# Kernel tuning notes

Hardware: AMD Instinct MI355X
Metric: run time of the kernel (lower is better)

## Reference

```python
import jax, jax.numpy as jnp
import numpy as np

N, E, L, HID, HEADS, G = 50000, 800000, 2, 128, 8, 256
DK = HID // HEADS

def _ln(x, g, b, eps=1e-5):
    m = jnp.mean(x, axis=-1, keepdims=True)
    v = jnp.mean((x - m) ** 2, axis=-1, keepdims=True)
    return (x - m) * jax.lax.rsqrt(v + eps) * g + b

def setup_inputs() -> dict:
    key = jax.random.key(0)
    ks = jax.random.split(key, 24)
    rn = lambda i, s: (0.05 * jax.random.normal(ks[i], s)).astype(jnp.float32)
    return {
        'node_attr': jax.random.randint(ks[0], (N, 4), 0, 64, dtype=jnp.int32),
        'batch_idx': jnp.sort(jax.random.randint(ks[1], (N,), 0, G, dtype=jnp.int32)),
        'edge_index': jax.random.randint(ks[2], (2, E), 0, N, dtype=jnp.int32),
        'strat_dist': jax.random.randint(ks[3], (E,), 0, 32, dtype=jnp.int32),
        'strat_path': jax.random.randint(ks[4], (E,), 0, 16, dtype=jnp.int32),
        'atom_emb': rn(5, (4, 64, HID)),
        'dist_emb': rn(6, (L, 32, HID)),
        'path_emb': rn(7, (L, 16, HID)),
        'Wq': rn(8, (L, HID, HID)), 'bq': rn(9, (L, HID)),
        'Wk': rn(10, (L, HID, HID)), 'bk': rn(11, (L, HID)),
        'Wv': rn(12, (L, HID, HID)), 'bv': rn(13, (L, HID)),
        'Wa': rn(14, (L, HID, HID)), 'ba': rn(15, (L, HID)),
        'ln1_g': jnp.ones((L, HID), jnp.float32), 'ln1_b': jnp.zeros((L, HID), jnp.float32),
        'Wmid': rn(16, (L, HID, 2 * HID)), 'bmid': rn(17, (L, 2 * HID)),
        'Wo': rn(18, (L, 2 * HID, HID)), 'bo': rn(19, (L, HID)),
        'ln2_g': jnp.ones((L, HID), jnp.float32), 'ln2_b': jnp.zeros((L, HID), jnp.float32),
        'W_out': rn(20, (HID, 1)), 'b_out': jnp.zeros((1,), jnp.float32),
    }

def reference(node_attr, batch_idx, edge_index, strat_dist, strat_path,
              atom_emb, dist_emb, path_emb, Wq, bq, Wk, bk, Wv, bv, Wa, ba,
              ln1_g, ln1_b, Wmid, bmid, Wo, bo, ln2_g, ln2_b, W_out, b_out):
    # node encoder: sum of per-feature embeddings (AtomEncoder style)
    x = sum(atom_emb[f][node_attr[:, f]] for f in range(node_attr.shape[1]))  # [N, HID]
    src, tgt = edge_index[0], edge_index[1]  # j (source), i (target)
    inv_sqrt_dk = np.float32(1.0 / np.sqrt(DK))
    for l in range(L):
        # per-edge gather + relational encodings added to the source vector
        s = x[src] + dist_emb[l][strat_dist] + path_emb[l][strat_path]  # [E, HID]
        t = x[tgt]                                                      # [E, HID]
        q = (t @ Wq[l] + bq[l]).reshape(E, HEADS, DK)
        k = (s @ Wk[l] + bk[l]).reshape(E, HEADS, DK)
        v = (s @ Wv[l] + bv[l]).reshape(E, HEADS, DK)
        scores = jnp.sum(q * k, axis=-1) * inv_sqrt_dk  # [E, HEADS]
        # segment softmax keyed on target node id
        smax = jax.ops.segment_max(scores, tgt, num_segments=N)
        ex = jnp.exp(scores - smax[tgt])
        den = jax.ops.segment_sum(ex, tgt, num_segments=N)
        att = ex / (den[tgt] + 1e-16)                   # [E, HEADS]
        msg = (v * att[:, :, None]).reshape(E, HID)
        aggr = jax.ops.segment_sum(msg, tgt, num_segments=N)  # scatter-add
        # update: attn FFN + residual + LayerNorms (dropout is identity in eval)
        h = _ln(jax.nn.gelu(aggr, approximate=False) @ Wa[l] + ba[l] + x, ln1_g[l], ln1_b[l])
        h2 = jax.nn.gelu(h @ Wmid[l] + bmid[l], approximate=False) @ Wo[l] + bo[l]
        x = _ln(h2 + h, ln2_g[l], ln2_b[l])
    # global mean pool per graph, then readout
    cnt = jax.ops.segment_sum(jnp.ones((N,), x.dtype), batch_idx, num_segments=G)
    pooled = jax.ops.segment_sum(x, batch_idx, num_segments=G) / jnp.maximum(cnt, 1.0)[:, None]
    return pooled @ W_out + b_out
```

## Files before the change

kernel.cpp:

```cpp
#include <hip/hip_runtime.h>
#include <hip/hip_bf16.h>
#include <math.h>
#include <stdint.h>

#define N_NODES 50000
#define N_EDGES 800000
#define HID 128
#define NGRAPH 256
#define NLAYER 2
#define CAP 64

#define SC_GRP 196
#define SC_B (SC_GRP * 8)
#define NPART 6250

#define ENC_B 3125
#define TKV_B (ENC_B + 1024)
#define RPK_B (TKV_B + 128)
#define PREP_B (RPK_B + 4)

#define PKE_B 782
#define PKZ_B 196
#define PACK_B (PKE_B + PKZ_B)

typedef __bf16 bf16x8 __attribute__((ext_vector_type(8)));
typedef __bf16 bf16x4 __attribute__((ext_vector_type(4)));
typedef __bf16 bf16x2 __attribute__((ext_vector_type(2)));
typedef float f32x4 __attribute__((ext_vector_type(4)));
typedef float f32x2 __attribute__((ext_vector_type(2)));

__device__ __forceinline__ float gelu_f(float v) {
    return 0.5f * v * (1.0f + erff(v * 0.70710678118654752f));
}

__device__ __forceinline__ f32x2 f8lo(uint32_t d) {
    return __builtin_amdgcn_cvt_pk_f32_fp8((int)d, false);
}
__device__ __forceinline__ f32x2 f8hi(uint32_t d) {
    return __builtin_amdgcn_cvt_pk_f32_fp8((int)d, true);
}
__device__ __forceinline__ uint32_t pk4_fp8(float a, float b, float c, float d) {
    int w = __builtin_amdgcn_cvt_pk_fp8_f32(a, b, 0, false);
    w = __builtin_amdgcn_cvt_pk_fp8_f32(c, d, w, true);
    return (uint32_t)w;
}
__device__ __forceinline__ f32x2 bfpair(uint32_t d) {
    f32x2 r;
    r[0] = __uint_as_float(d << 16);
    r[1] = __uint_as_float(d);
    return r;
}

__global__ __launch_bounds__(256) void pack_kernel(
    const int* __restrict__ tgt, const int* __restrict__ src,
    const int* __restrict__ sd, const int* __restrict__ sp,
    uint32_t* __restrict__ pack, uint16_t* __restrict__ t16,
    int* __restrict__ cnt) {
    int b = blockIdx.x;
    int tid = threadIdx.x;
    if (b < PKE_B) {
        int e0 = b * 1024 + tid * 4;
        if (e0 + 3 < N_EDGES) {
            int4 s4 = *(const int4*)(src + e0);
            int4 d4 = *(const int4*)(sd + e0);
            int4 p4 = *(const int4*)(sp + e0);
            int4 t4 = *(const int4*)(tgt + e0);
            uint4 o;
            o.x = (uint32_t)s4.x | ((uint32_t)((d4.x << 4) | p4.x) << 16);
            o.y = (uint32_t)s4.y | ((uint32_t)((d4.y << 4) | p4.y) << 16);
            o.z = (uint32_t)s4.z | ((uint32_t)((d4.z << 4) | p4.z) << 16);
            o.w = (uint32_t)s4.w | ((uint32_t)((d4.w << 4) | p4.w) << 16);
            *(uint4*)(pack + e0) = o;
            uint2 tt;
            tt.x = (uint32_t)t4.x | ((uint32_t)t4.y << 16);
            tt.y = (uint32_t)t4.z | ((uint32_t)t4.w << 16);
            *(uint2*)(t16 + e0) = tt;
        }
    } else {
        int idx = (b - PKE_B) * 256 + tid;
        if (idx < N_NODES) cnt[idx] = 0;
    }
}

__global__ __launch_bounds__(256) void prep_kernel(
    const int* __restrict__ attr, const float* __restrict__ aemb,
    __bf16* __restrict__ xb,
    const float* __restrict__ de, const float* __restrict__ pe,
    const float* __restrict__ Wk, const float* __restrict__ Wv,
    __bf16* __restrict__ tkv,
    const float* __restrict__ Wq, const float* __restrict__ Wa,
    const float* __restrict__ Wmid, const float* __restrict__ Wo,
    __bf16* __restrict__ wqkvf, __bf16* __restrict__ waf,
    __bf16* __restrict__ wmidf, __bf16* __restrict__ wof,
    const int* __restrict__ batch, const float* __restrict__ bout,
    const float* __restrict__ bq, const float* __restrict__ bk,
    const float* __restrict__ bv,
    float* __restrict__ invc, float* __restrict__ outp, float* __restrict__ bqkv,
    const uint16_t* __restrict__ t16, const uint32_t* __restrict__ pack,
    int* __restrict__ cnt, uint32_t* __restrict__ ei) {
    __shared__ float sde[128];
    int b = blockIdx.x;
    int tid = threadIdx.x;
    if (b < SC_B) {
        int grp = b >> 3;
        int part = b & 7;
        unsigned plo = (unsigned)(part * NPART);
        int base = grp * 4096 + tid;
#pragma unroll
        for (int k = 0; k < 16; k++) {
            int e = base + k * 256;
            if (e < N_EDGES) {
                unsigned tl = (unsigned)t16[e] - plo;
                if (tl < (unsigned)NPART) {
                    int t = (int)(tl + plo);
                    uint32_t pk = pack[e];
                    int r = atomicAdd(&cnt[t], 1);
                    if (r < CAP) ei[(t << 6) + r] = pk;
                }
            }
        }
        return;
    }
    b -= SC_B;
    if (b < ENC_B) {
        int gid = b * 256 + tid;
        int n = gid >> 4;
        int c8 = (gid & 15) << 3;
        const int4 a = *(const int4*)(attr + n * 4);
        const float* r0 = aemb + (size_t)(0 * 64 + a.x) * 128 + c8;
        const float* r1 = aemb + (size_t)(1 * 64 + a.y) * 128 + c8;
        const float* r2 = aemb + (size_t)(2 * 64 + a.z) * 128 + c8;
        const float* r3 = aemb + (size_t)(3 * 64 + a.w) * 128 + c8;
        f32x4 v0a = *(const f32x4*)r0, v0b = *(const f32x4*)(r0 + 4);
        f32x4 v1a = *(const f32x4*)r1, v1b = *(const f32x4*)(r1 + 4);
        f32x4 v2a = *(const f32x4*)r2, v2b = *(const f32x4*)(r2 + 4);
        f32x4 v3a = *(const f32x4*)r3, v3b = *(const f32x4*)(r3 + 4);
        bf16x8 o;
#pragma unroll
        for (int j = 0; j < 4; j++) {
            o[j] = (__bf16)(v0a[j] + v1a[j] + v2a[j] + v3a[j]);
            o[4 + j] = (__bf16)(v0b[j] + v1b[j] + v2b[j] + v3b[j]);
        }
        *(bf16x8*)(xb + (size_t)n * 128 + c8) = o;
    } else if (b < TKV_B) {
        int bb = b - ENC_B;
        int l = bb >> 9;
        int md = bb & 511;
        int dd = md >> 4, pp = md & 15;
        int c = tid;
        if (c < 128) sde[c] = de[l * 4096 + dd * 128 + c] + pe[l * 2048 + pp * 128 + c];
        __syncthreads();
        const float* W = (c < 128) ? (Wk + l * 16384) : (Wv + l * 16384);
        int cc = c & 127;
        float acc = 0.f;
#pragma unroll 4
        for (int k = 0; k < 128; k++) acc = fmaf(sde[k], W[k * 128 + cc], acc);
        tkv[(size_t)bb * 256 + c] = (__bf16)acc;
    } else if (b < RPK_B) {
        int u = (b - TKV_B) * 256 + tid;
        int l = u >> 14, r = u & 16383;
        const float* srcp;
        __bf16* dstp;
        int kg, scol, srcCO;
        if (r < 6144) {
            kg = r / 384;
            int uu = r % 384;
            int sec = uu >> 7, cc = uu & 127;
            scol = ((cc & 15) << 3) | (cc >> 4);
            const float* Ws = (sec == 0) ? Wq : (sec == 1) ? Wk : Wv;
            srcp = Ws + l * 16384;
            srcCO = 128;
            dstp = wqkvf + (size_t)l * 49152 + (size_t)r * 8;
        } else if (r < 8192) {
            int rr = r - 6144;
            kg = rr >> 7;
            int cc = rr & 127;
            scol = ((cc & 15) << 3) | (cc >> 4);
            srcp = Wa + l * 16384;
            srcCO = 128;
            dstp = waf + (size_t)l * 16384 + (size_t)rr * 8;
        } else if (r < 12288) {
            int rr = r - 8192;
            kg = rr >> 8;
            int uu = rr & 255;
            int blk = uu >> 7, cc = uu & 127;
            scol = blk * 128 + (((cc & 15) << 3) | (cc >> 4));
            srcp = Wmid + l * 32768;
            srcCO = 256;
            dstp = wmidf + (size_t)l * 32768 + (size_t)rr * 8;
        } else {
            int rr = r - 12288;
            kg = rr >> 7;
            int cc = rr & 127;
            scol = ((cc & 15) << 3) | (cc >> 4);
            srcp = Wo + l * 32768;
            srcCO = 128;
            dstp = wof + (size_t)l * 32768 + (size_t)rr * 8;
        }
        bf16x8 o;
#pragma unroll
        for (int j = 0; j < 8; j++) o[j] = (__bf16)srcp[(kg * 8 + j) * srcCO + scol];
        *(bf16x8*)dstp = o;
    } else {
        int sb = b - RPK_B;
        if (sb == 0) {
            int g = tid;
            int lo = 0, hi = N_NODES;
            while (lo < hi) { int mid = (lo + hi) >> 1; if (batch[mid] < g) lo = mid + 1; else hi = mid; }
            int start = lo;
            lo = start; hi = N_NODES;
            while (lo < hi) { int mid = (lo + hi) >> 1; if (batch[mid] < g + 1) lo = mid + 1; else hi = mid; }
            int c2 = lo - start;
            invc[g] = 1.0f / fmaxf((float)c2, 1.0f);
            outp[g] = bout[0];
        } else {
            int r = (sb - 1) * 256 + tid;
            int l = r / 384, c = r % 384;
            float v = (c < 128) ? bq[l * 128 + c]
                    : (c < 256) ? bk[l * 128 + c - 128]
                                : bv[l * 128 + c - 256];
            bqkv[r] = v;
        }
    }
}

__global__ __launch_bounds__(256) void qkv_gemm(
    const __bf16* __restrict__ A, const __bf16* __restrict__ Wf,
    const float* __restrict__ bias, __bf16* __restrict__ Qb,
    uint8_t* __restrict__ kv8, int M) {
    int tid = threadIdx.x;
    int bq = blockIdx.x;
    int sec = bq % 3;
    int rowblk = bq / 3;
    int lane = tid & 63;
    int wv = tid >> 6;
    int row0 = rowblk * 64 + wv * 16;
    int col0 = sec * 128;
    if (row0 >= M) return;
    int quad = lane >> 4, tq = lane & 15;
    f32x4 acc[8] = {};
#pragma unroll
    for (int k0 = 0; k0 < 128; k0 += 32) {
        int rr = row0 + tq;
        if (rr >= M) rr = M - 1;
        bf16x8 af = *(const bf16x8*)(A + (size_t)rr * 128 + k0 + quad * 8);
#pragma unroll
        for (int nt = 0; nt < 8; nt++) {
            bf16x8 bfr = *(const bf16x8*)(Wf + ((size_t)((k0 >> 3) + quad) * 384 + col0 + nt * 16 + tq) * 8);
            acc[nt] = __builtin_amdgcn_mfma_f32_16x16x32_bf16(af, bfr, acc[nt], 0, 0, 0);
        }
    }
    int cb = tq * 8;
    float bia[8];
#pragma unroll
    for (int t = 0; t < 8; t++) bia[t] = bias[col0 + cb + t];
#pragma unroll
    for (int v = 0; v < 4; v++) {
        int rr = row0 + quad * 4 + v;
        if (rr >= M) continue;
        float val[8];
#pragma unroll
        for (int t = 0; t < 8; t++) val[t] = acc[t][v] + bia[t];
        if (sec == 0) {
            bf16x8 ov;
#pragma unroll
            for (int t = 0; t < 8; t++) ov[t] = (__bf16)val[t];
            *(bf16x8*)(Qb + (size_t)rr * 128 + cb) = ov;
        } else {
            uint2 st;
            st.x = pk4_fp8(val[0], val[1], val[2], val[3]);
            st.y = pk4_fp8(val[4], val[5], val[6], val[7]);
            *(uint2*)(kv8 + (size_t)rr * 256 + (sec - 1) * 128 + cb) = st;
        }
    }
}

template <bool POOL>
__global__ __launch_bounds__(256) void ffn_uber(
    const __bf16* __restrict__ A,
    const __bf16* __restrict__ xres,
    const __bf16* __restrict__ Waf, const float* __restrict__ ba,
    const float* __restrict__ l1g, const float* __restrict__ l1b,
    const __bf16* __restrict__ Wmf, const float* __restrict__ bmid,
    const __bf16* __restrict__ Wof, const float* __restrict__ bo,
    const float* __restrict__ l2g, const float* __restrict__ l2b,
    __bf16* __restrict__ outx,
    const int* __restrict__ batch, const float* __restrict__ invc,
    const float* __restrict__ WoutV, float* __restrict__ outp,
    int M) {
    __shared__ __bf16 hld[4][16][136];
    __shared__ __bf16 smid[4][16][264];
    __shared__ float ps[POOL ? NGRAPH : 1];
    int lane = threadIdx.x & 63;
    int wv = threadIdx.x >> 6;
    int row0 = blockIdx.x * 64 + wv * 16;
    bool active = row0 < M;
    if (POOL) {
        ps[threadIdx.x] = 0.f;
        __syncthreads();
    } else if (!active) {
        return;
    }
    int quad = lane >> 4, tq = lane & 15;
    if (active) {
        int cb = tq * 8;
        {
            f32x4 acc[8] = {};
#pragma unroll
            for (int k0 = 0; k0 < 128; k0 += 32) {
                int rr = row0 + tq;
                if (rr >= M) rr = M - 1;
                bf16x8 af = *(const bf16x8*)(A + (size_t)rr * 128 + k0 + quad * 8);
#pragma unroll
                for (int nt = 0; nt < 8; nt++) {
                    bf16x8 bfr = *(const bf16x8*)(Waf + ((size_t)((k0 >> 3) + quad) * 128 + nt * 16 + tq) * 8);
                    acc[nt] = __builtin_amdgcn_mfma_f32_16x16x32_bf16(af, bfr, acc[nt], 0, 0, 0);
                }
            }
            float bia[8], gv[8], bv2[8];
#pragma unroll
            for (int t = 0; t < 8; t++) {
                bia[t] = ba[cb + t];
                gv[t] = l1g[cb + t];
                bv2[t] = l1b[cb + t];
            }
#pragma unroll
            for (int v = 0; v < 4; v++) {
                int rr = row0 + quad * 4 + v;
                int rc = (rr < M) ? rr : M - 1;
                bf16x8 rv = *(const bf16x8*)(xres + (size_t)rc * 128 + cb);
                float val[8];
#pragma unroll
                for (int t = 0; t < 8; t++) val[t] = acc[t][v] + bia[t] + (float)rv[t];
                float s = 0.f, s2 = 0.f;
#pragma unroll
                for (int t = 0; t < 8; t++) { s += val[t]; s2 = fmaf(val[t], val[t], s2); }
#pragma unroll
                for (int o = 1; o < 16; o <<= 1) {
                    s += __shfl_xor(s, o);
                    s2 += __shfl_xor(s2, o);
                }
                float m = s * (1.0f / 128.0f);
                float var = s2 * (1.0f / 128.0f) - m * m;
                float rs = rsqrtf(var + 1e-5f);
                bf16x8 ov;
#pragma unroll
                for (int t = 0; t < 8; t++) ov[t] = (__bf16)((val[t] - m) * rs * gv[t] + bv2[t]);
                *(bf16x8*)(&hld[wv][quad * 4 + v][cb]) = ov;
            }
        }
        asm volatile("" ::: "memory");
#pragma unroll
        for (int cH = 0; cH < 2; ++cH) {
            f32x4 acc[8] = {};
#pragma unroll
            for (int k0 = 0; k0 < 128; k0 += 32) {
                bf16x8 af = *(const bf16x8*)(&hld[wv][tq][k0 + quad * 8]);
#pragma unroll
                for (int nt = 0; nt < 8; nt++) {
                    bf16x8 bfr = *(const bf16x8*)(Wmf + ((size_t)((k0 >> 3) + quad) * 256 + cH * 128 + nt * 16 + tq) * 8);
                    acc[nt] = __builtin_amdgcn_mfma_f32_16x16x32_bf16(af, bfr, acc[nt], 0, 0, 0);
                }
            }
            int cb2 = cH * 128 + cb;
            float bia[8];
#pragma unroll
            for (int t = 0; t < 8; t++) bia[t] = bmid[cb2 + t];
#pragma unroll
            for (int v = 0; v < 4; v++) {
                bf16x8 ov;
#pragma unroll
                for (int t = 0; t < 8; t++) ov[t] = (__bf16)gelu_f(acc[t][v] + bia[t]);
                *(bf16x8*)(&smid[wv][quad * 4 + v][cb2]) = ov;
            }
        }
        asm volatile("" ::: "memory");
        f32x4 acc[8] = {};
#pragma unroll
        for (int k0 = 0; k0 < 256; k0 += 32) {
            bf16x8 af = *(const bf16x8*)(&smid[wv][tq][k0 + quad * 8]);
#pragma unroll
            for (int nt = 0; nt < 8; nt++) {
                bf16x8 bfr = *(const bf16x8*)(Wof + ((size_t)((k0 >> 3) + quad) * 128 + nt * 16 + tq) * 8);
                acc[nt] = __builtin_amdgcn_mfma_f32_16x16x32_bf16(af, bfr, acc[nt], 0, 0, 0);
            }
        }
        float bia[8], gv[8], bv2[8], wo8[8];
#pragma unroll
        for (int t = 0; t < 8; t++) {
            bia[t] = bo[cb + t];
            gv[t] = l2g[cb + t];
            bv2[t] = l2b[cb + t];
        }
        if (POOL) {
#pragma unroll
            for (int t = 0; t < 8; t++) wo8[t] = WoutV[cb + t];
        }
#pragma unroll
        for (int v = 0; v < 4; v++) {
            int rr = row0 + quad * 4 + v;
            bf16x8 rv = *(const bf16x8*)(&hld[wv][quad * 4 + v][cb]);
            float val[8];
#pragma unroll
            for (int t = 0; t < 8; t++) val[t] = acc[t][v] + bia[t] + (float)rv[t];
            float s = 0.f, s2 = 0.f;
#pragma unroll
            for (int t = 0; t < 8; t++) { s += val[t]; s2 = fmaf(val[t], val[t], s2); }
#pragma unroll
            for (int o = 1; o < 16; o <<= 1) {
                s += __shfl_xor(s, o);
                s2 += __shfl_xor(s2, o);
            }
            float m = s * (1.0f / 128.0f);
            float var = s2 * (1.0f / 128.0f) - m * m;
            float rs = rsqrtf(var + 1e-5f);
#pragma unroll
            for (int t = 0; t < 8; t++) val[t] = (val[t] - m) * rs * gv[t] + bv2[t];
            if (rr >= M) continue;
            if (!POOL) {
                bf16x8 ov;
#pragma unroll
                for (int t = 0; t < 8; t++) ov[t] = (__bf16)val[t];
                *(bf16x8*)(outx + (size_t)rr * 128 + cb) = ov;
            } else {
                float dot = 0.f;
#pragma unroll
                for (int t = 0; t < 8; t++) dot = fmaf(val[t], wo8[t], dot);
#pragma unroll
                for (int o = 1; o < 16; o <<= 1) dot += __shfl_xor(dot, o);
                if (tq == 0) {
                    int g = batch[rr];
                    atomicAdd(&ps[g], dot * invc[g]);
                }
            }
        }
    }
    if (POOL) {
        __syncthreads();
        float pv = ps[threadIdx.x];
        if (pv != 0.f) atomicAdd(&outp[threadIdx.x], pv);
    }
}

__global__ __launch_bounds__(256) void attn_kernel(
    const __bf16* __restrict__ Qb, const uint8_t* __restrict__ kv8,
    const __bf16* __restrict__ tkv,
    const int* __restrict__ cnt, const uint32_t* __restrict__ ei,
    __bf16* __restrict__ outb) {
    int wv = threadIdx.x >> 6;
    int lane = threadIdx.x & 63;
    int nd = lane >> 5;
    int slot = (lane >> 3) & 3;
    int h = lane & 7;
    int i = blockIdx.x * 8 + wv * 2 + nd;
    int ch0 = h * 16;
    const uint4* qv = (const uint4*)(Qb + (size_t)i * 128 + ch0);
    uint4 qa = qv[0], qb = qv[1];
    uint32_t qd[8] = {qa.x, qa.y, qa.z, qa.w, qb.x, qb.y, qb.z, qb.w};
    f32x2 qp[8];
#pragma unroll
    for (int j = 0; j < 8; j++) qp[j] = bfpair(qd[j]);
    int deg = cnt[i];
    if (deg > CAP) deg = CAP;
    int p0 = i << 6;
    int p1 = p0 + deg;
    float l = 0.f;
    f32x2 ap[8] = {};
    int p = p0 + slot;
    uint32_t w1 = 0, w2 = 0;
    if (p < p1) w1 = ei[p];
    if (p + 4 < p1) w2 = ei[p + 4];
    uint4 kw, vw, t0, t1, u0, u1;
    {
        int j = w1 & 0xffff, md = w1 >> 16;
        const uint8_t* kr = kv8 + (size_t)j * 256 + ch0;
        kw = *(const uint4*)kr;
        vw = *(const uint4*)(kr + 128);
        const __bf16* tr = tkv + md * 256 + ch0;
        t0 = *(const uint4*)tr;
        t1 = *(const uint4*)(tr + 8);
        u0 = *(const uint4*)(tr + 128);
        u1 = *(const uint4*)(tr + 136);
    }
    while (p < p1) {
        uint4 kwn, vwn, t0n, t1n, u0n, u1n;
        {
            int j = w2 & 0xffff, md = w2 >> 16;
            const uint8_t* kr = kv8 + (size_t)j * 256 + ch0;
            kwn = *(const uint4*)kr;
            vwn = *(const uint4*)(kr + 128);
            const __bf16* tr = tkv + md * 256 + ch0;
            t0n = *(const uint4*)tr;
            t1n = *(const uint4*)(tr + 8);
            u0n = *(const uint4*)(tr + 128);
            u1n = *(const uint4*)(tr + 136);
        }
        int pn = p + 8;
        uint32_t w3 = ei[(pn < p1) ? pn : p0];
        uint32_t kd[4] = {kw.x, kw.y, kw.z, kw.w};
        uint32_t vd[4] = {vw.x, vw.y, vw.z, vw.w};
        uint32_t td[8] = {t0.x, t0.y, t0.z, t0.w, t1.x, t1.y, t1.z, t1.w};
        uint32_t ud[8] = {u0.x, u0.y, u0.z, u0.w, u1.x, u1.y, u1.z, u1.w};
        f32x2 sa = {0.f, 0.f};
#pragma unroll
        for (int j = 0; j < 4; j++) {
            f32x2 klo = f8lo(kd[j]) + bfpair(td[2 * j]);
            f32x2 khi = f8hi(kd[j]) + bfpair(td[2 * j + 1]);
            sa = qp[2 * j] * klo + sa;
            sa = qp[2 * j + 1] * khi + sa;
        }
        float s = sa[0] + sa[1];
        float pe = __expf(s * 0.25f);
        l += pe;
        f32x2 pp = {pe, pe};
#pragma unroll
        for (int j = 0; j < 4; j++) {
            f32x2 vlo = f8lo(vd[j]) + bfpair(ud[2 * j]);
            f32x2 vhi = f8hi(vd[j]) + bfpair(ud[2 * j + 1]);
            ap[2 * j] = pp * vlo + ap[2 * j];
            ap[2 * j + 1] = pp * vhi + ap[2 * j + 1];
        }
        kw = kwn; vw = vwn; t0 = t0n; t1 = t1n; u0 = u0n; u1 = u1n;
        w2 = w3;
        p += 4;
    }
#pragma unroll
    for (int m = 8; m <= 16; m <<= 1) {
        l += __shfl_xor(l, m);
#pragma unroll
        for (int j = 0; j < 8; j++) {
            f32x2 o;
            o[0] = __shfl_xor(ap[j][0], m);
            o[1] = __shfl_xor(ap[j][1], m);
            ap[j] = ap[j] + o;
        }
    }
    float inv = 1.0f / (l + 1e-16f);
    f32x2 va = ap[0], vb = ap[1];
    if (slot == 1) { va = ap[2]; vb = ap[3]; }
    if (slot == 2) { va = ap[4]; vb = ap[5]; }
    if (slot == 3) { va = ap[6]; vb = ap[7]; }
    bf16x4 o4;
    o4[0] = (__bf16)gelu_f(va[0] * inv);
    o4[1] = (__bf16)gelu_f(va[1] * inv);
    o4[2] = (__bf16)gelu_f(vb[0] * inv);
    o4[3] = (__bf16)gelu_f(vb[1] * inv);
    *(bf16x4*)(outb + (size_t)i * 128 + ch0 + slot * 4) = o4;
}

extern "C" void kernel_launch(void* const* d_in, const int* in_sizes, int n_in,
                              void* d_out, int out_size, void* d_ws, size_t ws_size,
                              hipStream_t stream) {
    const int N = N_NODES, E = N_EDGES;
    const int* node_attr = (const int*)d_in[0];
    const int* batch_idx = (const int*)d_in[1];
    const int* edge_index = (const int*)d_in[2];
    const int* strat_dist = (const int*)d_in[3];
    const int* strat_path = (const int*)d_in[4];
    const float* atom_emb = (const float*)d_in[5];
    const float* dist_emb = (const float*)d_in[6];
    const float* path_emb = (const float*)d_in[7];
    const float* Wq = (const float*)d_in[8];
    const float* bq = (const float*)d_in[9];
    const float* Wk = (const float*)d_in[10];
    const float* bk = (const float*)d_in[11];
    const float* Wv = (const float*)d_in[12];
    const float* bv = (const float*)d_in[13];
    const float* Wa = (const float*)d_in[14];
    const float* ba = (const float*)d_in[15];
    const float* ln1g = (const float*)d_in[16];
    const float* ln1b = (const float*)d_in[17];
    const float* Wmid = (const float*)d_in[18];
    const float* bmid = (const float*)d_in[19];
    const float* Wo = (const float*)d_in[20];
    const float* bo = (const float*)d_in[21];
    const float* ln2g = (const float*)d_in[22];
    const float* ln2b = (const float*)d_in[23];
    const float* Wout = (const float*)d_in[24];
    const float* bout = (const float*)d_in[25];
    float* out = (float*)d_out;

    const int* src = edge_index;
    const int* tgt = edge_index + E;

    size_t NF = (size_t)N * HID;
    float* invc = (float*)d_ws;
    float* bqkv = invc + 256;
    __bf16* xb = (__bf16*)(bqkv + 768);
    __bf16* Qb = xb + NF;
    __bf16* ab = Qb + NF;
    __bf16* tkv = ab + NF;
    __bf16* wqkvf = tkv + 262144;
    __bf16* waf = wqkvf + 98304;
    __bf16* wmidf = waf + 32768;
    __bf16* wof = wmidf + 65536;
    uint8_t* kv8 = (uint8_t*)(wof + 65536);
    uint32_t* ei = (uint32_t*)(kv8 + (size_t)N * 256);
    int* cnt = (int*)(ei + (size_t)N * CAP);
    uint32_t* pack = (uint32_t*)(cnt + N_NODES);
    uint16_t* t16 = (uint16_t*)(pack + N_EDGES);

    pack_kernel<<<PACK_B, 256, 0, stream>>>(
        tgt, src, strat_dist, strat_path, pack, t16, cnt);
    prep_kernel<<<SC_B + PREP_B, 256, 0, stream>>>(
        node_attr, atom_emb, xb,
        dist_emb, path_emb, Wk, Wv, tkv,
        Wq, Wa, Wmid, Wo, wqkvf, waf, wmidf, wof,
        batch_idx, bout, bq, bk, bv, invc, out, bqkv,
        t16, pack, cnt, ei);

    const int GB = (N + 63) / 64;
    const int AB = (N + 7) / 8;

    for (int l = 0; l < NLAYER; ++l) {
        qkv_gemm<<<3 * GB, 256, 0, stream>>>(
            xb, wqkvf + l * 49152, bqkv + l * 384, Qb, kv8, N);

        attn_kernel<<<AB, 256, 0, stream>>>(Qb, kv8, tkv + l * 131072, cnt, ei, ab);

        if (l < NLAYER - 1) {
            ffn_uber<false><<<GB, 256, 0, stream>>>(
                ab, xb, waf + l * 16384, ba + l * 128, ln1g + l * 128, ln1b + l * 128,
                wmidf + l * 32768, bmid + l * 256, wof + l * 32768, bo + l * 128,
                ln2g + l * 128, ln2b + l * 128, xb,
                nullptr, nullptr, nullptr, nullptr, N);
        } else {
            ffn_uber<true><<<GB, 256, 0, stream>>>(
                ab, xb, waf + l * 16384, ba + l * 128, ln1g + l * 128, ln1b + l * 128,
                wmidf + l * 32768, bmid + l * 256, wof + l * 32768, bo + l * 128,
                ln2g + l * 128, ln2b + l * 128, nullptr,
                batch_idx, invc, Wout, out, N);
        }
    }
}
```

Measured before the change: 412.8 us.

## Assign one wavefront per node in attention with 8 edge slots and butterfly reduce

The attention kernel now maps one 64-lane wavefront to each target node instead of two nodes per wavefront, so 8 edge slots per node are processed in parallel instead of 4. The cross-slot reduction becomes a recursive-halving butterfly that exchanges half the accumulators per step, ending with each lane owning two output channels, which cuts shuffle count. This doubles the grid size and halves the per-lane loop trip count for high-degree nodes, at the cost of more idle lanes on low-degree nodes (average degree is around 16).

```diff
diff --git a/kernel.cpp b/kernel.cpp
--- a/kernel.cpp
+++ b/kernel.cpp
@@ -24,7 +24,6 @@
 #define PACK_B (PKE_B + PKZ_B)
 
 typedef __bf16 bf16x8 __attribute__((ext_vector_type(8)));
-typedef __bf16 bf16x4 __attribute__((ext_vector_type(4)));
 typedef __bf16 bf16x2 __attribute__((ext_vector_type(2)));
 typedef float f32x4 __attribute__((ext_vector_type(4)));
 typedef float f32x2 __attribute__((ext_vector_type(2)));
@@ -48,6 +47,12 @@
     f32x2 r;
     r[0] = __uint_as_float(d << 16);
     r[1] = __uint_as_float(d);
+    return r;
+}
+__device__ __forceinline__ f32x2 shfl2(f32x2 v, int m) {
+    f32x2 r;
+    r[0] = __shfl_xor(v[0], m);
+    r[1] = __shfl_xor(v[1], m);
     return r;
 }
 
@@ -448,11 +453,9 @@
     const int* __restrict__ cnt, const uint32_t* __restrict__ ei,
     __bf16* __restrict__ outb) {
     int wv = threadIdx.x >> 6;
+    int i = blockIdx.x * 4 + wv;
     int lane = threadIdx.x & 63;
-    int nd = lane >> 5;
-    int slot = (lane >> 3) & 3;
-    int h = lane & 7;
-    int i = blockIdx.x * 8 + wv * 2 + nd;
+    int slot = lane >> 3, h = lane & 7;
     int ch0 = h * 16;
     const uint4* qv = (const uint4*)(Qb + (size_t)i * 128 + ch0);
     uint4 qa = qv[0], qb = qv[1];
@@ -469,7 +472,7 @@
     int p = p0 + slot;
     uint32_t w1 = 0, w2 = 0;
     if (p < p1) w1 = ei[p];
-    if (p + 4 < p1) w2 = ei[p + 4];
+    if (p + 8 < p1) w2 = ei[p + 8];
     uint4 kw, vw, t0, t1, u0, u1;
     {
         int j = w1 & 0xffff, md = w1 >> 16;
@@ -495,8 +498,8 @@
             u0n = *(const uint4*)(tr + 128);
             u1n = *(const uint4*)(tr + 136);
         }
-        int pn = p + 8;
-        uint32_t w3 = ei[(pn < p1) ? pn : p0];
+        int pn = p + 16;
+        uint32_t w3 = ei[(pn < p1) ? pn : p];
         uint32_t kd[4] = {kw.x, kw.y, kw.z, kw.w};
         uint32_t vd[4] = {vw.x, vw.y, vw.z, vw.w};
         uint32_t td[8] = {t0.x, t0.y, t0.z, t0.w, t1.x, t1.y, t1.z, t1.w};
@@ -522,30 +525,40 @@
         }
         kw = kwn; vw = vwn; t0 = t0n; t1 = t1n; u0 = u0n; u1 = u1n;
         w2 = w3;
-        p += 4;
-    }
-#pragma unroll
-    for (int m = 8; m <= 16; m <<= 1) {
-        l += __shfl_xor(l, m);
-#pragma unroll
-        for (int j = 0; j < 8; j++) {
-            f32x2 o;
-            o[0] = __shfl_xor(ap[j][0], m);
-            o[1] = __shfl_xor(ap[j][1], m);
-            ap[j] = ap[j] + o;
-        }
+        p += 8;
+    }
+    int b3 = (lane >> 3) & 1, b4 = (lane >> 4) & 1, b5 = lane >> 5;
+    f32x2 k0, k1, k2, k3;
+    {
+        f32x2 s0 = b3 ? ap[0] : ap[1];
+        f32x2 s1 = b3 ? ap[2] : ap[3];
+        f32x2 s2 = b3 ? ap[4] : ap[5];
+        f32x2 s3 = b3 ? ap[6] : ap[7];
+        k0 = (b3 ? ap[1] : ap[0]) + shfl2(s0, 8);
+        k1 = (b3 ? ap[3] : ap[2]) + shfl2(s1, 8);
+        k2 = (b3 ? ap[5] : ap[4]) + shfl2(s2, 8);
+        k3 = (b3 ? ap[7] : ap[6]) + shfl2(s3, 8);
+        l += __shfl_xor(l, 8);
+    }
+    f32x2 m0, m1;
+    {
+        f32x2 s0 = b4 ? k0 : k1;
+        f32x2 s1 = b4 ? k2 : k3;
+        m0 = (b4 ? k1 : k0) + shfl2(s0, 16);
+        m1 = (b4 ? k3 : k2) + shfl2(s1, 16);
+        l += __shfl_xor(l, 16);
+    }
+    f32x2 fin;
+    {
+        f32x2 s0 = b5 ? m0 : m1;
+        fin = (b5 ? m1 : m0) + shfl2(s0, 32);
+        l += __shfl_xor(l, 32);
     }
     float inv = 1.0f / (l + 1e-16f);
-    f32x2 va = ap[0], vb = ap[1];
-    if (slot == 1) { va = ap[2]; vb = ap[3]; }
-    if (slot == 2) { va = ap[4]; vb = ap[5]; }
-    if (slot == 3) { va = ap[6]; vb = ap[7]; }
-    bf16x4 o4;
-    o4[0] = (__bf16)gelu_f(va[0] * inv);
-    o4[1] = (__bf16)gelu_f(va[1] * inv);
-    o4[2] = (__bf16)gelu_f(vb[0] * inv);
-    o4[3] = (__bf16)gelu_f(vb[1] * inv);
-    *(bf16x4*)(outb + (size_t)i * 128 + ch0 + slot * 4) = o4;
+    bf16x2 o2;
+    o2[0] = (__bf16)gelu_f(fin[0] * inv);
+    o2[1] = (__bf16)gelu_f(fin[1] * inv);
+    *(bf16x2*)(outb + (size_t)i * 128 + ch0 + slot * 2) = o2;
 }
 
 extern "C" void kernel_launch(void* const* d_in, const int* in_sizes, int n_in,
@@ -610,7 +623,7 @@
         t16, pack, cnt, ei);
 
     const int GB = (N + 63) / 64;
-    const int AB = (N + 7) / 8;
+    const int AB = (N + 3) / 4;
 
     for (int l = 0; l < NLAYER; ++l) {
         qkv_gemm<<<3 * GB, 256, 0, stream>>>(
```

After: 372.6 us. 1.11x faster.

## Fuse node encoding with layer-0 QKV GEMM and widen attention per-node wave

Applied to the files above, without the earlier changes.

Weight repacking and setup move into the pack kernel. The node encoder now stages each 64-node tile in shared memory and computes the layer-0 Q/K/V projection with MFMA inside the same prep kernel, which removes the first qkv_gemm launch and the re-read of x. The attention kernel now assigns one full wave per target node instead of half a wave, and processes 8 edges per step with an extra shuffle-reduction stage. The ENCQ blocks depend on repacked weights, so the prep kernel must run after the pack kernel. Some encoder blocks now carry heavy GEMM work while the scatter blocks are light, which risks load imbalance.

```diff
diff --git a/kernel.cpp b/kernel.cpp
--- a/kernel.cpp
+++ b/kernel.cpp
@@ -14,17 +14,17 @@
 #define SC_B (SC_GRP * 8)
 #define NPART 6250
 
-#define ENC_B 3125
-#define TKV_B (ENC_B + 1024)
-#define RPK_B (TKV_B + 128)
-#define PREP_B (RPK_B + 4)
+#define ENCQ_B 782
+#define TKV_B 1024
+#define PREPM_B (SC_B + ENCQ_B + TKV_B)
 
 #define PKE_B 782
 #define PKZ_B 196
-#define PACK_B (PKE_B + PKZ_B)
+#define RPK0 (PKE_B + PKZ_B)
+#define SET0 (RPK0 + 128)
+#define PACK_B (SET0 + 4)
 
 typedef __bf16 bf16x8 __attribute__((ext_vector_type(8)));
-typedef __bf16 bf16x4 __attribute__((ext_vector_type(4)));
 typedef __bf16 bf16x2 __attribute__((ext_vector_type(2)));
 typedef float f32x4 __attribute__((ext_vector_type(4)));
 typedef float f32x2 __attribute__((ext_vector_type(2)));
@@ -55,7 +55,16 @@
     const int* __restrict__ tgt, const int* __restrict__ src,
     const int* __restrict__ sd, const int* __restrict__ sp,
     uint32_t* __restrict__ pack, uint16_t* __restrict__ t16,
-    int* __restrict__ cnt) {
+    int* __restrict__ cnt,
+    const float* __restrict__ Wq, const float* __restrict__ Wa,
+    const float* __restrict__ Wmid, const float* __restrict__ Wo,
+    const float* __restrict__ Wk, const float* __restrict__ Wv,
+    __bf16* __restrict__ wqkvf, __bf16* __restrict__ waf,
+    __bf16* __restrict__ wmidf, __bf16* __restrict__ wof,
+    const int* __restrict__ batch, const float* __restrict__ bout,
+    const float* __restrict__ bq, const float* __restrict__ bk,
+    const float* __restrict__ bv,
+    float* __restrict__ invc, float* __restrict__ outp, float* __restrict__ bqkv) {
     int b = blockIdx.x;
     int tid = threadIdx.x;
     if (b < PKE_B) {
@@ -76,88 +85,11 @@
             tt.y = (uint32_t)t4.z | ((uint32_t)t4.w << 16);
             *(uint2*)(t16 + e0) = tt;
         }
-    } else {
+    } else if (b < RPK0) {
         int idx = (b - PKE_B) * 256 + tid;
         if (idx < N_NODES) cnt[idx] = 0;
-    }
-}
-
-__global__ __launch_bounds__(256) void prep_kernel(
-    const int* __restrict__ attr, const float* __restrict__ aemb,
-    __bf16* __restrict__ xb,
-    const float* __restrict__ de, const float* __restrict__ pe,
-    const float* __restrict__ Wk, const float* __restrict__ Wv,
-    __bf16* __restrict__ tkv,
-    const float* __restrict__ Wq, const float* __restrict__ Wa,
-    const float* __restrict__ Wmid, const float* __restrict__ Wo,
-    __bf16* __restrict__ wqkvf, __bf16* __restrict__ waf,
-    __bf16* __restrict__ wmidf, __bf16* __restrict__ wof,
-    const int* __restrict__ batch, const float* __restrict__ bout,
-    const float* __restrict__ bq, const float* __restrict__ bk,
-    const float* __restrict__ bv,
-    float* __restrict__ invc, float* __restrict__ outp, float* __restrict__ bqkv,
-    const uint16_t* __restrict__ t16, const uint32_t* __restrict__ pack,
-    int* __restrict__ cnt, uint32_t* __restrict__ ei) {
-    __shared__ float sde[128];
-    int b = blockIdx.x;
-    int tid = threadIdx.x;
-    if (b < SC_B) {
-        int grp = b >> 3;
-        int part = b & 7;
-        unsigned plo = (unsigned)(part * NPART);
-        int base = grp * 4096 + tid;
-#pragma unroll
-        for (int k = 0; k < 16; k++) {
-            int e = base + k * 256;
-            if (e < N_EDGES) {
-                unsigned tl = (unsigned)t16[e] - plo;
-                if (tl < (unsigned)NPART) {
-                    int t = (int)(tl + plo);
-                    uint32_t pk = pack[e];
-                    int r = atomicAdd(&cnt[t], 1);
-                    if (r < CAP) ei[(t << 6) + r] = pk;
-                }
-            }
-        }
-        return;
-    }
-    b -= SC_B;
-    if (b < ENC_B) {
-        int gid = b * 256 + tid;
-        int n = gid >> 4;
-        int c8 = (gid & 15) << 3;
-        const int4 a = *(const int4*)(attr + n * 4);
-        const float* r0 = aemb + (size_t)(0 * 64 + a.x) * 128 + c8;
-        const float* r1 = aemb + (size_t)(1 * 64 + a.y) * 128 + c8;
-        const float* r2 = aemb + (size_t)(2 * 64 + a.z) * 128 + c8;
-        const float* r3 = aemb + (size_t)(3 * 64 + a.w) * 128 + c8;
-        f32x4 v0a = *(const f32x4*)r0, v0b = *(const f32x4*)(r0 + 4);
-        f32x4 v1a = *(const f32x4*)r1, v1b = *(const f32x4*)(r1 + 4);
-        f32x4 v2a = *(const f32x4*)r2, v2b = *(const f32x4*)(r2 + 4);
-        f32x4 v3a = *(const f32x4*)r3, v3b = *(const f32x4*)(r3 + 4);
-        bf16x8 o;
-#pragma unroll
-        for (int j = 0; j < 4; j++) {
-            o[j] = (__bf16)(v0a[j] + v1a[j] + v2a[j] + v3a[j]);
-            o[4 + j] = (__bf16)(v0b[j] + v1b[j] + v2b[j] + v3b[j]);
-        }
-        *(bf16x8*)(xb + (size_t)n * 128 + c8) = o;
-    } else if (b < TKV_B) {
-        int bb = b - ENC_B;
-        int l = bb >> 9;
-        int md = bb & 511;
-        int dd = md >> 4, pp = md & 15;
-        int c = tid;
-        if (c < 128) sde[c] = de[l * 4096 + dd * 128 + c] + pe[l * 2048 + pp * 128 + c];
-        __syncthreads();
-        const float* W = (c < 128) ? (Wk + l * 16384) : (Wv + l * 16384);
-        int cc = c & 127;
-        float acc = 0.f;
-#pragma unroll 4
-        for (int k = 0; k < 128; k++) acc = fmaf(sde[k], W[k * 128 + cc], acc);
-        tkv[(size_t)bb * 256 + c] = (__bf16)acc;
-    } else if (b < RPK_B) {
-        int u = (b - TKV_B) * 256 + tid;
+    } else if (b < SET0) {
+        int u = (b - RPK0) * 256 + tid;
         int l = u >> 14, r = u & 16383;
         const float* srcp;
         __bf16* dstp;
@@ -202,7 +134,7 @@
         for (int j = 0; j < 8; j++) o[j] = (__bf16)srcp[(kg * 8 + j) * srcCO + scol];
         *(bf16x8*)dstp = o;
     } else {
-        int sb = b - RPK_B;
+        int sb = b - SET0;
         if (sb == 0) {
             int g = tid;
             int lo = 0, hi = N_NODES;
@@ -221,6 +153,127 @@
                                 : bv[l * 128 + c - 256];
             bqkv[r] = v;
         }
+    }
+}
+
+__global__ __launch_bounds__(256) void prep_mega(
+    const int* __restrict__ attr, const float* __restrict__ aemb,
+    __bf16* __restrict__ xb,
+    const float* __restrict__ de, const float* __restrict__ pe,
+    const float* __restrict__ Wk, const float* __restrict__ Wv,
+    __bf16* __restrict__ tkv,
+    const __bf16* __restrict__ wqkvf, const float* __restrict__ bqkv,
+    __bf16* __restrict__ Qb, uint8_t* __restrict__ kv8,
+    const uint16_t* __restrict__ t16, const uint32_t* __restrict__ pack,
+    int* __restrict__ cnt, uint32_t* __restrict__ ei) {
+    __shared__ __bf16 xt[64][136];
+    __shared__ float sde[128];
+    int b = blockIdx.x;
+    int tid = threadIdx.x;
+    if (b < SC_B) {
+        int grp = b >> 3;
+        int part = b & 7;
+        unsigned plo = (unsigned)(part * NPART);
+        int base = grp * 4096 + tid;
+#pragma unroll
+        for (int k = 0; k < 16; k++) {
+            int e = base + k * 256;
+            if (e < N_EDGES) {
+                unsigned tl = (unsigned)t16[e] - plo;
+                if (tl < (unsigned)NPART) {
+                    int t = (int)(tl + plo);
+                    uint32_t pk = pack[e];
+                    int r = atomicAdd(&cnt[t], 1);
+                    if (r < CAP) ei[(t << 6) + r] = pk;
+                }
+            }
+        }
+        return;
+    }
+    b -= SC_B;
+    if (b < ENCQ_B) {
+        int n0 = b * 64;
+#pragma unroll
+        for (int it = 0; it < 4; ++it) {
+            int task = it * 256 + tid;
+            int nl = task >> 4;
+            int c8 = (task & 15) << 3;
+            int n = n0 + nl;
+            int nc = (n < N_NODES) ? n : N_NODES - 1;
+            const int4 a = *(const int4*)(attr + (size_t)nc * 4);
+            const float* r0 = aemb + (size_t)a.x * 128 + c8;
+            const float* r1 = aemb + (size_t)(64 + a.y) * 128 + c8;
+            const float* r2 = aemb + (size_t)(128 + a.z) * 128 + c8;
+            const float* r3 = aemb + (size_t)(192 + a.w) * 128 + c8;
+            f32x4 v0a = *(const f32x4*)r0, v0b = *(const f32x4*)(r0 + 4);
+            f32x4 v1a = *(const f32x4*)r1, v1b = *(const f32x4*)(r1 + 4);
+            f32x4 v2a = *(const f32x4*)r2, v2b = *(const f32x4*)(r2 + 4);
+            f32x4 v3a = *(const f32x4*)r3, v3b = *(const f32x4*)(r3 + 4);
+            bf16x8 o;
+#pragma unroll
+            for (int j = 0; j < 4; j++) {
+                o[j] = (__bf16)(v0a[j] + v1a[j] + v2a[j] + v3a[j]);
+                o[4 + j] = (__bf16)(v0b[j] + v1b[j] + v2b[j] + v3b[j]);
+            }
+            *(bf16x8*)(&xt[nl][c8]) = o;
+            if (n < N_NODES) *(bf16x8*)(xb + (size_t)n * 128 + c8) = o;
+        }
+        __syncthreads();
+        int lane = tid & 63;
+        int wv = tid >> 6;
+        int quad = lane >> 4, tq = lane & 15;
+        int row0 = n0 + wv * 16;
+        int cb = tq * 8;
+#pragma unroll
+        for (int sec = 0; sec < 3; ++sec) {
+            int col0 = sec * 128;
+            f32x4 acc[8] = {};
+#pragma unroll
+            for (int k0 = 0; k0 < 128; k0 += 32) {
+                bf16x8 af = *(const bf16x8*)(&xt[wv * 16 + tq][k0 + quad * 8]);
+#pragma unroll
+                for (int nt = 0; nt < 8; nt++) {
+                    bf16x8 bfr = *(const bf16x8*)(wqkvf + ((size_t)((k0 >> 3) + quad) * 384 + col0 + nt * 16 + tq) * 8);
+                    acc[nt] = __builtin_amdgcn_mfma_f32_16x16x32_bf16(af, bfr, acc[nt], 0, 0, 0);
+                }
+            }
+            float bia[8];
+#pragma unroll
+            for (int t = 0; t < 8; t++) bia[t] = bqkv[col0 + cb + t];
+#pragma unroll
+            for (int v = 0; v < 4; v++) {
+                int rr = row0 + quad * 4 + v;
+                if (rr >= N_NODES) continue;
+                float val[8];
+#pragma unroll
+                for (int t = 0; t < 8; t++) val[t] = acc[t][v] + bia[t];
+                if (sec == 0) {
+                    bf16x8 ov;
+#pragma unroll
+                    for (int t = 0; t < 8; t++) ov[t] = (__bf16)val[t];
+                    *(bf16x8*)(Qb + (size_t)rr * 128 + cb) = ov;
+                } else {
+                    uint2 st;
+                    st.x = pk4_fp8(val[0], val[1], val[2], val[3]);
+                    st.y = pk4_fp8(val[4], val[5], val[6], val[7]);
+                    *(uint2*)(kv8 + (size_t)rr * 256 + (sec - 1) * 128 + cb) = st;
+                }
+            }
+        }
+    } else {
+        int bb = b - ENCQ_B;
+        int l = bb >> 9;
+        int md = bb & 511;
+        int dd = md >> 4, pp = md & 15;
+        int c = tid;
+        if (c < 128) sde[c] = de[l * 4096 + dd * 128 + c] + pe[l * 2048 + pp * 128 + c];
+        __syncthreads();
+        const float* W = (c < 128) ? (Wk + l * 16384) : (Wv + l * 16384);
+        int cc = c & 127;
+        float acc = 0.f;
+#pragma unroll 4
+        for (int k = 0; k < 128; k++) acc = fmaf(sde[k], W[k * 128 + cc], acc);
+        tkv[(size_t)bb * 256 + c] = (__bf16)acc;
     }
 }
 
@@ -448,11 +501,9 @@
     const int* __restrict__ cnt, const uint32_t* __restrict__ ei,
     __bf16* __restrict__ outb) {
     int wv = threadIdx.x >> 6;
+    int i = blockIdx.x * 4 + wv;
     int lane = threadIdx.x & 63;
-    int nd = lane >> 5;
-    int slot = (lane >> 3) & 3;
-    int h = lane & 7;
-    int i = blockIdx.x * 8 + wv * 2 + nd;
+    int slot = lane >> 3, h = lane & 7;
     int ch0 = h * 16;
     const uint4* qv = (const uint4*)(Qb + (size_t)i * 128 + ch0);
     uint4 qa = qv[0], qb = qv[1];
@@ -469,7 +520,7 @@
     int p = p0 + slot;
     uint32_t w1 = 0, w2 = 0;
     if (p < p1) w1 = ei[p];
-    if (p + 4 < p1) w2 = ei[p + 4];
+    if (p + 8 < p1) w2 = ei[p + 8];
     uint4 kw, vw, t0, t1, u0, u1;
     {
         int j = w1 & 0xffff, md = w1 >> 16;
@@ -495,8 +546,8 @@
             u0n = *(const uint4*)(tr + 128);
             u1n = *(const uint4*)(tr + 136);
         }
-        int pn = p + 8;
-        uint32_t w3 = ei[(pn < p1) ? pn : p0];
+        int pn = p + 16;
+        uint32_t w3 = ei[(pn < p1) ? pn : p];
         uint32_t kd[4] = {kw.x, kw.y, kw.z, kw.w};
         uint32_t vd[4] = {vw.x, vw.y, vw.z, vw.w};
         uint32_t td[8] = {t0.x, t0.y, t0.z, t0.w, t1.x, t1.y, t1.z, t1.w};
@@ -522,10 +573,10 @@
         }
         kw = kwn; vw = vwn; t0 = t0n; t1 = t1n; u0 = u0n; u1 = u1n;
         w2 = w3;
-        p += 4;
-    }
-#pragma unroll
-    for (int m = 8; m <= 16; m <<= 1) {
+        p += 8;
+    }
+#pragma unroll
+    for (int m = 8; m <= 32; m <<= 1) {
         l += __shfl_xor(l, m);
 #pragma unroll
         for (int j = 0; j < 8; j++) {
@@ -536,16 +587,15 @@
         }
     }
     float inv = 1.0f / (l + 1e-16f);
-    f32x2 va = ap[0], vb = ap[1];
-    if (slot == 1) { va = ap[2]; vb = ap[3]; }
-    if (slot == 2) { va = ap[4]; vb = ap[5]; }
-    if (slot == 3) { va = ap[6]; vb = ap[7]; }
-    bf16x4 o4;
-    o4[0] = (__bf16)gelu_f(va[0] * inv);
-    o4[1] = (__bf16)gelu_f(va[1] * inv);
-    o4[2] = (__bf16)gelu_f(vb[0] * inv);
-    o4[3] = (__bf16)gelu_f(vb[1] * inv);
-    *(bf16x4*)(outb + (size_t)i * 128 + ch0 + slot * 4) = o4;
+    float v0 = ap[0][0], v1 = ap[0][1];
+#pragma unroll
+    for (int j = 1; j < 8; j++) {
+        if (slot == j) { v0 = ap[j][0]; v1 = ap[j][1]; }
+    }
+    bf16x2 o2;
+    o2[0] = (__bf16)gelu_f(v0 * inv);
+    o2[1] = (__bf16)gelu_f(v1 * inv);
+    *(bf16x2*)(outb + (size_t)i * 128 + ch0 + slot * 2) = o2;
 }
 
 extern "C" void kernel_launch(void* const* d_in, const int* in_sizes, int n_in,
@@ -601,35 +651,29 @@
     uint16_t* t16 = (uint16_t*)(pack + N_EDGES);
 
     pack_kernel<<<PACK_B, 256, 0, stream>>>(
-        tgt, src, strat_dist, strat_path, pack, t16, cnt);
-    prep_kernel<<<SC_B + PREP_B, 256, 0, stream>>>(
-        node_attr, atom_emb, xb,
-        dist_emb, path_emb, Wk, Wv, tkv,
-        Wq, Wa, Wmid, Wo, wqkvf, waf, wmidf, wof,
-        batch_idx, bout, bq, bk, bv, invc, out, bqkv,
+        tgt, src, strat_dist, strat_path, pack, t16, cnt,
+        Wq, Wa, Wmid, Wo, Wk, Wv, wqkvf, waf, wmidf, wof,
+        batch_idx, bout, bq, bk, bv, invc, out, bqkv);
+    prep_mega<<<PREPM_B, 256, 0, stream>>>(
+        node_attr, atom_emb, xb, dist_emb, path_emb, Wk, Wv, tkv,
+        wqkvf, bqkv, Qb, kv8,
         t16, pack, cnt, ei);
 
     const int GB = (N + 63) / 64;
-    const int AB = (N + 7) / 8;
-
-    for (int l = 0; l < NLAYER; ++l) {
-        qkv_gemm<<<3 * GB, 256, 0, stream>>>(
-            xb, wqkvf + l * 49152, bqkv + l * 384, Qb, kv8, N);
-
-        attn_kernel<<<AB, 256, 0, stream>>>(Qb, kv8, tkv + l * 131072, cnt, ei, ab);
-
-        if (l < NLAYER - 1) {
-            ffn_uber<false><<<GB, 256, 0, stream>>>(
-                ab, xb, waf + l * 16384, ba + l * 128, ln1g + l * 128, ln1b + l * 128,
-                wmidf + l * 32768, bmid + l * 256, wof + l * 32768, bo + l * 128,
-                ln2g + l * 128, ln2b + l * 128, xb,
-                nullptr, nullptr, nullptr, nullptr, N);
-        } else {
-            ffn_uber<true><<<GB, 256, 0, stream>>>(
-                ab, xb, waf + l * 16384, ba + l * 128, ln1g + l * 128, ln1b + l * 128,
-                wmidf + l * 32768, bmid + l * 256, wof + l * 32768, bo + l * 128,
-                ln2g + l * 128, ln2b + l * 128, nullptr,
-                batch_idx, invc, Wout, out, N);
-        }
-    }
-}
+    const int AB = (N + 3) / 4;
+
+    attn_kernel<<<AB, 256, 0, stream>>>(Qb, kv8, tkv, cnt, ei, ab);
+    ffn_uber<false><<<GB, 256, 0, stream>>>(
+        ab, xb, waf, ba, ln1g, ln1b,
+        wmidf, bmid, wof, bo, ln2g, ln2b, xb,
+        nullptr, nullptr, nullptr, nullptr, N);
+
+    qkv_gemm<<<3 * GB, 256, 0, stream>>>(
+        xb, wqkvf + 49152, bqkv + 384, Qb, kv8, N);
+    attn_kernel<<<AB, 256, 0, stream>>>(Qb, kv8, tkv + 131072, cnt, ei, ab);
+    ffn_uber<true><<<GB, 256, 0, stream>>>(
+        ab, xb, waf + 16384, ba + 128, ln1g + 128, ln1b + 128,
+        wmidf + 32768, bmid + 256, wof + 32768, bo + 128, ln2g + 128, ln2b + 128,
+        nullptr,
+        batch_idx, invc, Wout, out, N);
+}
```

New measurement: 376.9 us. -8.7%, faster.
